# Kernel optimization log

Measured on AMD Instinct MI355X. Metric: run time of the kernel, lower is better.

Reference implementation:

```python
import jax, jax.numpy as jnp
import numpy as np

N_HEADS = 8
FACTOR = 5
N_LAYERS = 2
D_MODEL = 512


def _pos_enc(L, d):
    pos = jnp.arange(L, dtype=jnp.float32)[:, None]
    div = jnp.exp(jnp.arange(0, d, 2, dtype=jnp.float32) * (-np.log(10000.0) / d))
    pe = jnp.zeros((L, d), dtype=jnp.float32)
    pe = pe.at[:, 0::2].set(jnp.sin(pos * div))
    pe = pe.at[:, 1::2].set(jnp.cos(pos * div))
    return pe


def _ln(x, g, b, eps=1e-5):
    mu = x.mean(-1, keepdims=True)
    var = ((x - mu) ** 2).mean(-1, keepdims=True)
    return (x - mu) * jax.lax.rsqrt(var + eps) * g + b


def _token_conv(x, W):
    # x: [B, L, C_in]; W: [d_model, C_in, 3]; circular padding k=3 (Informer TokenEmbedding)
    xt = jnp.transpose(x, (0, 2, 1))
    xt = jnp.concatenate([xt[:, :, -1:], xt, xt[:, :, :1]], axis=-1)
    y = jax.lax.conv_general_dilated(xt, W, (1,), 'VALID', dimension_numbers=('NCH', 'OIH', 'NCH'))
    return jnp.transpose(y, (0, 2, 1))


def _prob_attention(Q, K, V):
    # ProbSparse attention (Informer). Q,K,V: [B,H,L,D]
    B, H, L, D = Q.shape
    ln_L = int(np.ceil(np.log(L)))
    U_part = min(FACTOR * ln_L, L)  # sampled keys per query
    u = min(FACTOR * ln_L, L)       # top queries kept
    idx = jax.random.randint(jax.random.key(42), (L, U_part), 0, L)  # shared across B,H as in torch
    K_sample = K[:, :, idx, :]                                  # [B,H,L,U_part,D]
    QK_sample = jnp.einsum('bhld,bhlud->bhlu', Q, K_sample)
    M = QK_sample.max(-1) - QK_sample.mean(-1)                  # sparsity measure [B,H,L]
    _, M_top = jax.lax.top_k(M, u)                              # [B,H,u]
    Q_reduce = jnp.take_along_axis(Q, M_top[..., None], axis=2) # [B,H,u,D]
    scores = jnp.einsum('bhud,bhld->bhul', Q_reduce, K) / jnp.sqrt(jnp.float32(D))
    attn = jax.nn.softmax(scores, axis=-1)
    ctx = jnp.broadcast_to(V.mean(axis=2, keepdims=True), Q.shape)  # non-selected -> mean(V)
    upd = jnp.einsum('bhul,bhld->bhud', attn, V)
    bi = jnp.arange(B)[:, None, None]
    hi = jnp.arange(H)[None, :, None]
    return ctx.at[bi, hi, M_top].set(upd)                       # scatter selected queries


def reference(x_state_enc, x_enc, x_mark_enc, state_emb_W, token_conv_W, time_W, time_b,
              Wq, bq, Wk, bk, Wv, bv, Wo, bo, ln1_g, ln1_b, ln2_g, ln2_b,
              ffn1_W, ffn1_b, ffn2_W, ffn2_b, norm_g, norm_b):
    B, L = x_state_enc.shape
    dm = D_MODEL
    H = N_HEADS
    dk = dm // H
    # StatePosEmbedding: state emb + token conv emb + time-feature linear + sinusoidal pos
    x = state_emb_W[x_state_enc] + _token_conv(x_enc, token_conv_W) + x_mark_enc @ time_W + time_b + _pos_enc(L, dm)
    for l in range(N_LAYERS):
        q = (x @ Wq[l] + bq[l]).reshape(B, L, H, dk).transpose(0, 2, 1, 3)
        k = (x @ Wk[l] + bk[l]).reshape(B, L, H, dk).transpose(0, 2, 1, 3)
        v = (x @ Wv[l] + bv[l]).reshape(B, L, H, dk).transpose(0, 2, 1, 3)
        ctx = _prob_attention(q, k, v).transpose(0, 2, 1, 3).reshape(B, L, dm)
        x = x + (ctx @ Wo[l] + bo[l])
        x = _ln(x, ln1_g[l], ln1_b[l])
        y = jax.nn.gelu(x @ ffn1_W[l] + ffn1_b[l], approximate=False)
        y = y @ ffn2_W[l] + ffn2_b[l]
        x = _ln(x + y, ln2_g[l], ln2_b[l])
    x = _ln(x, norm_g, norm_b)
    logits = x[:, -1:, :] @ state_emb_W.T  # pred_len = 1
    return logits[:, :, :-1]


def setup_inputs() -> dict:
    key = jax.random.key(0)
    ks = jax.random.split(key, 16)
    B, L, C_IN, MARK = 4, 2048, 7, 4
    NG = 100
    dm, dff, NL = 512, 2048, 2
    s = 0.02
    return {
        'x_state_enc': jax.random.randint(ks[0], (B, L), 0, NG + 1),
        'x_enc': jax.random.normal(ks[1], (B, L, C_IN), dtype=jnp.float32),
        'x_mark_enc': jax.random.normal(ks[2], (B, L, MARK), dtype=jnp.float32),
        'state_emb_W': jax.random.normal(ks[3], (NG + 1, dm), dtype=jnp.float32) * s,
        'token_conv_W': jax.random.normal(ks[4], (dm, C_IN, 3), dtype=jnp.float32) * s,
        'time_W': jax.random.normal(ks[5], (MARK, dm), dtype=jnp.float32) * s,
        'time_b': jnp.zeros((dm,), jnp.float32),
        'Wq': jax.random.normal(ks[6], (NL, dm, dm), dtype=jnp.float32) * s,
        'bq': jnp.zeros((NL, dm), jnp.float32),
        'Wk': jax.random.normal(ks[7], (NL, dm, dm), dtype=jnp.float32) * s,
        'bk': jnp.zeros((NL, dm), jnp.float32),
        'Wv': jax.random.normal(ks[8], (NL, dm, dm), dtype=jnp.float32) * s,
        'bv': jnp.zeros((NL, dm), jnp.float32),
        'Wo': jax.random.normal(ks[9], (NL, dm, dm), dtype=jnp.float32) * s,
        'bo': jnp.zeros((NL, dm), jnp.float32),
        'ln1_g': jnp.ones((NL, dm), jnp.float32),
        'ln1_b': jnp.zeros((NL, dm), jnp.float32),
        'ln2_g': jnp.ones((NL, dm), jnp.float32),
        'ln2_b': jnp.zeros((NL, dm), jnp.float32),
        'ffn1_W': jax.random.normal(ks[10], (NL, dm, dff), dtype=jnp.float32) * s,
        'ffn1_b': jnp.zeros((NL, dff), jnp.float32),
        'ffn2_W': jax.random.normal(ks[11], (NL, dff, dm), dtype=jnp.float32) * s,
        'ffn2_b': jnp.zeros((NL, dm), jnp.float32),
        'norm_g': jnp.ones((dm,), jnp.float32),
        'norm_b': jnp.zeros((dm,), jnp.float32),
    }
```

## Files before the change

kernel.cpp:

```cpp
#include <hip/hip_runtime.h>
#include <hip/hip_bf16.h>

#define L_SEQ 2048
#define NB    4
#define DM    512
#define NH    8
#define DK    64
#define DFF   2048
#define NSAMP 40
#define NGRID 100
#define PARTC 16
#define CKEY  128

typedef __attribute__((ext_vector_type(8))) short bf16x8;
typedef __attribute__((ext_vector_type(4))) float f32x4;

__device__ __forceinline__ unsigned rotl32(unsigned x, unsigned r){ return (x<<r)|(x>>(32u-r)); }
__device__ __forceinline__ float bf2f(ushort u){ return __uint_as_float(((unsigned)u)<<16); }
__device__ __forceinline__ ushort f2bf(float f){
  unsigned u = __float_as_uint(f);
  unsigned r = (u + 0x7fffu + ((u>>16)&1u)) >> 16;
  return (ushort)r;
}

__device__ __forceinline__ void threefry2x32(unsigned k0, unsigned k1, unsigned x0, unsigned x1,
                                             unsigned &o0, unsigned &o1){
  unsigned ks0=k0, ks1=k1, ks2=k0^k1^0x1BD11BDAu;
  x0 += ks0; x1 += ks1;
#define RND(r) { x0 += x1; x1 = rotl32(x1, r); x1 ^= x0; }
  RND(13u) RND(15u) RND(26u) RND(6u)   x0+=ks1; x1+=ks2+1u;
  RND(17u) RND(29u) RND(16u) RND(24u)  x0+=ks2; x1+=ks0+2u;
  RND(13u) RND(15u) RND(26u) RND(6u)   x0+=ks0; x1+=ks1+3u;
  RND(17u) RND(29u) RND(16u) RND(24u)  x0+=ks1; x1+=ks2+4u;
  RND(13u) RND(15u) RND(26u) RND(6u)   x0+=ks2; x1+=ks0+5u;
#undef RND
  o0=x0; o1=x1;
}

__global__ __launch_bounds__(256) void k_prep(
    const float* __restrict__ Wq, const float* __restrict__ Wk,
    const float* __restrict__ Wv, const float* __restrict__ Wo,
    const float* __restrict__ f1W, const float* __restrict__ f2W,
    const float* __restrict__ bq, const float* __restrict__ bk, const float* __restrict__ bv,
    ushort* __restrict__ wt, float* __restrict__ bcat, int* __restrict__ sidx)
{
  const size_t F1T=1048576, F2T=2097152, LSTR=3145728;
  int bid = blockIdx.x, t = threadIdx.x;
  if (bid >= 6145){
    int i = (bid-6145)*256 + t;
    const int total = L_SEQ*NSAMP;
    if (i < total){
      unsigned o0, o1;
      threefry2x32(0u, 42u, 0u, (unsigned)(total + i), o0, o1);
      sidx[i] = (int)((o0 ^ o1) & (unsigned)(L_SEQ-1));
    }
    return;
  }
  if (bid == 6144){
    for (int i=t; i<2*1536; i+=256){
      int l = i / 1536, r = i - l*1536;
      float v = (r<512) ? bq[l*DM+r] : (r<1024) ? bk[l*DM+r-512] : bv[l*DM+r-1024];
      bcat[i] = v;
    }
    return;
  }
  int l = bid >= 3072; bid -= l*3072;
  const float* src; ushort* dst; int K, N, tile;
  if (bid < 1024){
    int m = bid >> 8; tile = bid & 255;
    src = (m==0?Wq:m==1?Wk:m==2?Wv:Wo) + (size_t)l*DM*DM;
    dst = wt + (size_t)l*LSTR + (size_t)m*262144; K=DM; N=DM;
  } else if (bid < 2048){
    tile = bid-1024; src = f1W + (size_t)l*DM*DFF; dst = wt + (size_t)l*LSTR + F1T; K=DM; N=DFF;
  } else {
    tile = bid-2048; src = f2W + (size_t)l*DFF*DM; dst = wt + (size_t)l*LSTR + F2T; K=DFF; N=DM;
  }
  int ntn = N/32;
  int n0 = (tile % ntn)*32, k0 = (tile / ntn)*32;
  __shared__ float tl[32][33];
  int r = t >> 5, c = t & 31;
  for (int rr=r; rr<32; rr+=8) tl[rr][c] = src[(size_t)(k0+rr)*N + n0 + c];
  __syncthreads();
  for (int rr=r; rr<32; rr+=8)
    dst[(size_t)(n0+rr)*K + k0 + c] = f2bf(tl[c][rr]);
}

__global__ __launch_bounds__(256) void k_embed(const int* __restrict__ tok,
    const float* __restrict__ x_enc, const float* __restrict__ x_mark,
    const float* __restrict__ embW, const float* __restrict__ convW,
    const float* __restrict__ timeW, const float* __restrict__ timeb,
    float* __restrict__ x, ushort* __restrict__ xb){
  int bl = blockIdx.x; int b = bl >> 11; int l = bl & (L_SEQ-1);
  __shared__ float xin[21];
  __shared__ float xm[4];
  int t = threadIdx.x;
  if (t < 21){
    int tt = t/7, i = t - tt*7;
    int ll = (l + tt - 1) & (L_SEQ-1);
    xin[t] = x_enc[((size_t)b*L_SEQ + ll)*7 + i];
  }
  if (t >= 32 && t < 36) xm[t-32] = x_mark[((size_t)b*L_SEQ + l)*4 + (t-32)];
  __syncthreads();
  int tk = tok[bl];
  #pragma unroll
  for (int rep=0; rep<2; rep++){
    int d = t + rep*256;
    float v = embW[(size_t)tk*DM + d];
    const float* w = convW + (size_t)d*21;
    float cv = 0.f;
    #pragma unroll
    for (int tt=0; tt<3; tt++)
      #pragma unroll
      for (int i=0; i<7; i++)
        cv = fmaf(xin[tt*7+i], w[i*3+tt], cv);
    v += cv;
    float tv = timeb[d];
    #pragma unroll
    for (int m=0; m<4; m++) tv = fmaf(xm[m], timeW[m*DM + d], tv);
    v += tv;
    int j = d >> 1;
    float div = expf((float)(2*j) * (-0.017988946039015984f));
    float ang = (float)l * div;
    v += (d & 1) ? cosf(ang) : sinf(ang);
    x[(size_t)bl*DM + d] = v;
    xb[(size_t)bl*DM + d] = f2bf(v);
  }
}

enum { MG_ADD=0, MG_GELU_BF16=1, MG_QKV=2 };

__global__ __launch_bounds__(256) void k_mgemm(
    const ushort* __restrict__ A, const ushort* __restrict__ Bt,
    const float* __restrict__ bias, float* __restrict__ Cf,
    ushort* __restrict__ Cb, int M, int N, int K, int mode)
{
  __shared__ ushort As[64][64];
  __shared__ ushort Bs[64][64];
  int tid = threadIdx.x, lane = tid & 63, wid = tid >> 6;
  int nwg = gridDim.x*gridDim.y;
  int id  = blockIdx.y*gridDim.x + blockIdx.x;
  int sid = (id & 7)*(nwg >> 3) + (id >> 3);
  int bx = sid % gridDim.x, by = sid / gridDim.x;
  int m0 = by*64, n0 = bx*64;
  int wr = wid >> 1, wc = wid & 1;
  f32x4 acc[2][2];
  #pragma unroll
  for (int i=0;i<2;i++)
    #pragma unroll
    for(int j=0;j<2;j++) acc[i][j] = (f32x4){0.f,0.f,0.f,0.f};

  for (int k0 = 0; k0 < K; k0 += 64){
    __syncthreads();
    #pragma unroll
    for (int it=0; it<2; it++){
      int e   = it*256 + tid;
      int row = e >> 3, seg = e & 7;
      int gseg = seg ^ (row & 7);
      __builtin_amdgcn_global_load_lds(
        (const __attribute__((address_space(1))) void*)(A + (size_t)(m0+row)*K + k0 + gseg*8),
        (__attribute__((address_space(3))) void*)(&As[0][0] + (size_t)e*8), 16, 0, 0);
      __builtin_amdgcn_global_load_lds(
        (const __attribute__((address_space(1))) void*)(Bt + (size_t)(n0+row)*K + k0 + gseg*8),
        (__attribute__((address_space(3))) void*)(&Bs[0][0] + (size_t)e*8), 16, 0, 0);
    }
    __syncthreads();
    #pragma unroll
    for (int kk=0; kk<2; kk++){
      bf16x8 af[2], bfv[2];
      int seg = kk*4 + (lane>>4);
      #pragma unroll
      for (int i=0;i<2;i++){
        int row = wr*32 + i*16 + (lane&15);
        af[i]  = *(const bf16x8*)&As[row][(seg ^ (row&7))*8];
      }
      #pragma unroll
      for (int j=0;j<2;j++){
        int row = wc*32 + j*16 + (lane&15);
        bfv[j] = *(const bf16x8*)&Bs[row][(seg ^ (row&7))*8];
      }
      #pragma unroll
      for (int i=0;i<2;i++)
        #pragma unroll
        for (int j=0;j<2;j++)
          acc[i][j] = __builtin_amdgcn_mfma_f32_16x16x32_bf16(af[i], bfv[j], acc[i][j], 0,0,0);
    }
  }

  int fq = lane >> 4, fr = lane & 15;
  for (int i=0;i<2;i++){
    for (int j=0;j<2;j++){
      #pragma unroll
      for (int jj=0;jj<4;jj++){
        int r = m0 + wr*32 + i*16 + fq*4 + jj;
        int c = n0 + wc*32 + j*16 + fr;
        float v = acc[i][j][jj] + bias[c];
        if (mode == MG_ADD){
          Cf[(size_t)r*N + c] += v;
        } else if (mode == MG_GELU_BF16){
          float g = 0.5f*v*(1.f + erff(v*0.70710678118654752f));
          Cb[(size_t)r*N + c] = f2bf(g);
        } else {
          int b = r >> 11, l = r & (L_SEQ-1), m3 = c >> 9, hh = (c>>6)&7, d = c & 63;
          Cb[(size_t)m3*4194304 + (((size_t)b*NH + hh)*L_SEQ + l)*64 + d] = f2bf(v);
        }
      }
    }
  }
}

__global__ __launch_bounds__(256) void k_vmean1(const ushort* __restrict__ V, float* __restrict__ part){
  int blk = blockIdx.x;
  int bh = blk >> 5, ch = blk & 31;
  int t = threadIdx.x, d = t & 63, c = t >> 6;
  const ushort* Vb = V + (size_t)bh*L_SEQ*DK + (size_t)(ch*64 + c*16)*DK;
  float s = 0.f;
  #pragma unroll
  for (int r=0; r<16; r++) s += bf2f(Vb[r*DK + d]);
  __shared__ float red[256];
  red[t]=s; __syncthreads();
  if (t < 64) part[(size_t)blk*64 + t] = red[t]+red[t+64]+red[t+128]+red[t+192];
}
__global__ __launch_bounds__(64) void k_vmean2(const float* __restrict__ part, float* __restrict__ vmean){
  int bh = blockIdx.x, d = threadIdx.x;
  float s = 0.f;
  #pragma unroll
  for (int ch=0; ch<32; ch++) s += part[(size_t)(bh*32+ch)*64 + d];
  vmean[bh*64+d] = s * (1.f/(float)L_SEQ);
}

__global__ __launch_bounds__(256) void k_mscore(const ushort* __restrict__ Q, const ushort* __restrict__ Km,
    const int* __restrict__ idx, float* __restrict__ M){
  int wid = threadIdx.x >> 6, lane = threadIdx.x & 63;
  int g = blockIdx.x*4 + wid;
  int l = g & (L_SEQ-1), bh = g >> 11;
  int sg = lane >> 3, dg = lane & 7;

  bf16x8 qv = *(const bf16x8*)(Q + (size_t)g*64 + dg*8);
  float qf[8];
  #pragma unroll
  for (int e=0;e<8;e++) qf[e] = bf2f((ushort)qv[e]);

  const int* ir = idx + l*NSAMP;
  int ki[5];
  #pragma unroll
  for (int i=0;i<5;i++) ki[i] = ir[i*8 + sg];
  const ushort* Kb = Km + (size_t)bh*L_SEQ*64;
  bf16x8 kv[5];
  #pragma unroll
  for (int i=0;i<5;i++) kv[i] = *(const bf16x8*)(Kb + (size_t)ki[i]*64 + dg*8);

  float mx = -INFINITY, sm = 0.f;
  #pragma unroll
  for (int i=0;i<5;i++){
    float d = 0.f;
    #pragma unroll
    for (int e=0;e<8;e++) d = fmaf(qf[e], bf2f((ushort)kv[i][e]), d);
    #pragma unroll
    for (int off=1; off<8; off<<=1) d += __shfl_xor(d, off);
    mx = fmaxf(mx, d);
    sm += d;
  }
  #pragma unroll
  for (int off=1; off<64; off<<=1){
    mx = fmaxf(mx, __shfl_xor(mx, off));
    sm += __shfl_xor(sm, off);
  }
  if (lane==0) M[g] = mx - sm * (1.f/(8.f*(float)NSAMP));
}

__global__ __launch_bounds__(64) void k_topk(const float* __restrict__ M, int* __restrict__ Mtop){
  int bh = blockIdx.x, lane = threadIdx.x;
  float v[32];
  #pragma unroll
  for (int s=0; s<32; s++) v[s] = M[(size_t)bh*L_SEQ + s*64 + lane];
  for (int sel=0; sel<NSAMP; sel++){
    float best = -INFINITY; int bs = 0;
    #pragma unroll
    for (int s=0; s<32; s++){
      if (v[s] > best){ best = v[s]; bs = s; }
    }
    int bidx = bs*64 + lane;
    #pragma unroll
    for (int off=1; off<64; off<<=1){
      float ov = __shfl_xor(best, off);
      int   oi = __shfl_xor(bidx, off);
      if (ov > best || (ov == best && oi < bidx)){ best = ov; bidx = oi; }
    }
    if (lane == 0) Mtop[bh*NSAMP + sel] = bidx;
    int cs = bidx >> 6, cl = bidx & 63;
    if (lane == cl){
      #pragma unroll
      for (int s=0; s<32; s++) if (s == cs) v[s] = -INFINITY;
    }
  }
}

__global__ __launch_bounds__(256) void k_ctxfill(const float* __restrict__ vmean, ushort* __restrict__ ctx){
  int i = blockIdx.x*256 + threadIdx.x;
  int c = i & (DM-1);
  int b = i >> 20;
  int h = c >> 6, d = c & 63;
  ctx[i] = f2bf(vmean[((b<<3)+h)*64 + d]);
}

__global__ __launch_bounds__(256) void k_attn1(const ushort* __restrict__ Q, const ushort* __restrict__ K,
    const ushort* __restrict__ V, const int* __restrict__ Mtop,
    float* __restrict__ pm, float* __restrict__ ps, float* __restrict__ pO){
  int bid = blockIdx.x;
  int xcd = bid & 7, idx = bid >> 3;
  int bh = xcd*4 + (idx & 3), ch = idx >> 2;
  int l0 = ch * CKEY;
  int t = threadIdx.x, lane = t & 63, w = t >> 6;

  __shared__ ushort Qs[48][64];
  __shared__ ushort Ks[CKEY][64];
  __shared__ ushort Vs[CKEY][66];
  __shared__ ushort Ps[48][136];
  __shared__ float rmax[4][48];
  __shared__ float rsum[4][48];
  __shared__ float Oacc[48][64];
  __shared__ int qidx[48];

  if (t < 40) qidx[t] = Mtop[bh*NSAMP + t];
  const ushort* Kb = K + ((size_t)bh*L_SEQ + l0)*64;
  #pragma unroll
  for (int i=0;i<4;i++){
    int e = i*256 + t;
    __builtin_amdgcn_global_load_lds(
      (const __attribute__((address_space(1))) void*)(Kb + (size_t)e*8),
      (__attribute__((address_space(3))) void*)(&Ks[0][0] + (size_t)e*8), 16, 0, 0);
  }
  __syncthreads();

  const ushort* Qb = Q + (size_t)bh*L_SEQ*64;
  {
    int row = t >> 3, seg = t & 7;
    bf16x8 qv = *(const bf16x8*)(Qb + (size_t)qidx[row]*64 + seg*8);
    *(bf16x8*)&Qs[row][seg*8] = qv;
    if (t < 128){
      int r2 = 32 + (t>>3);
      bf16x8 z = (bf16x8){0,0,0,0,0,0,0,0};
      if (r2 < 40) z = *(const bf16x8*)(Qb + (size_t)qidx[r2]*64 + (t&7)*8);
      *(bf16x8*)&Qs[r2][(t&7)*8] = z;
    }
  }
  const ushort* Vb = V + ((size_t)bh*L_SEQ + l0)*64;
  #pragma unroll
  for (int i=0;i<4;i++){
    int e = i*256 + t;
    int row = e >> 3, seg = e & 7;
    bf16x8 vv = *(const bf16x8*)(Vb + (size_t)e*8);
    *(bf16x8*)&Vs[row][seg*8] = vv;
  }
  __syncthreads();

  for (int i=t; i<48*64; i+=256) ((float*)Oacc)[i] = 0.f;

  f32x4 sa[3][2];
  #pragma unroll
  for (int i=0;i<3;i++) for (int j=0;j<2;j++) sa[i][j] = (f32x4){0.f,0.f,0.f,0.f};
  #pragma unroll
  for (int ks=0; ks<2; ks++){
    int ko = ks*32 + (lane>>4)*8;
    bf16x8 af[3], bf[2];
    #pragma unroll
    for (int i=0;i<3;i++) af[i] = *(const bf16x8*)&Qs[i*16 + (lane&15)][ko];
    #pragma unroll
    for (int j=0;j<2;j++) bf[j] = *(const bf16x8*)&Ks[w*32 + j*16 + (lane&15)][ko];
    #pragma unroll
    for (int i=0;i<3;i++)
      #pragma unroll
      for (int j=0;j<2;j++)
        sa[i][j] = __builtin_amdgcn_mfma_f32_16x16x32_bf16(af[i], bf[j], sa[i][j], 0,0,0);
  }
  #pragma unroll
  for (int i=0;i<3;i++)
    #pragma unroll
    for (int j=0;j<2;j++)
      #pragma unroll
      for (int jj=0;jj<4;jj++) sa[i][j][jj] *= 0.125f;
  #pragma unroll
  for (int i=0;i<3;i++){
    #pragma unroll
    for (int jj=0;jj<4;jj++){
      float mx = fmaxf(sa[i][0][jj], sa[i][1][jj]);
      #pragma unroll
      for (int off=1; off<16; off<<=1) mx = fmaxf(mx, __shfl_xor(mx, off));
      if ((lane&15)==0) rmax[w][i*16 + (lane>>4)*4 + jj] = mx;
    }
  }
  __syncthreads();
  #pragma unroll
  for (int i=0;i<3;i++){
    #pragma unroll
    for (int jj=0;jj<4;jj++){
      int row = i*16 + (lane>>4)*4 + jj;
      float m = fmaxf(fmaxf(rmax[0][row], rmax[1][row]), fmaxf(rmax[2][row], rmax[3][row]));
      float p0 = __expf(sa[i][0][jj] - m);
      float p1 = __expf(sa[i][1][jj] - m);
      Ps[row][w*32 + (lane&15)]      = f2bf(p0);
      Ps[row][w*32 + 16 + (lane&15)] = f2bf(p1);
      float sm = p0 + p1;
      #pragma unroll
      for (int off=1; off<16; off<<=1) sm += __shfl_xor(sm, off);
      if ((lane&15)==0) rsum[w][row] = sm;
    }
  }
  __syncthreads();

  f32x4 oa[3][4];
  #pragma unroll
  for (int i=0;i<3;i++) for (int j=0;j<4;j++) oa[i][j] = (f32x4){0.f,0.f,0.f,0.f};
  {
    bf16x8 pa[3], vb[4];
    int kbase = w*32 + (lane>>4)*8;
    #pragma unroll
    for (int i=0;i<3;i++) pa[i] = *(const bf16x8*)&Ps[i*16 + (lane&15)][kbase];
    #pragma unroll
    for (int j=0;j<4;j++){
      #pragma unroll
      for (int e=0;e<8;e++) vb[j][e] = (short)Vs[kbase + e][j*16 + (lane&15)];
    }
    #pragma unroll
    for (int i=0;i<3;i++)
      #pragma unroll
      for (int j=0;j<4;j++)
        oa[i][j] = __builtin_amdgcn_mfma_f32_16x16x32_bf16(pa[i], vb[j], oa[i][j], 0,0,0);
  }
  #pragma unroll
  for (int ww=0; ww<4; ww++){
    if (w == ww){
      #pragma unroll
      for (int i=0;i<3;i++)
        #pragma unroll
        for (int j=0;j<4;j++)
          #pragma unroll
          for (int jj=0;jj<4;jj++)
            Oacc[i*16 + (lane>>4)*4 + jj][j*16 + (lane&15)] += oa[i][j][jj];
    }
    __syncthreads();
  }

  size_t base = ((size_t)bh*PARTC + ch);
  if (t < 40){
    float m = fmaxf(fmaxf(rmax[0][t], rmax[1][t]), fmaxf(rmax[2][t], rmax[3][t]));
    pm[base*40 + t] = m;
    ps[base*40 + t] = rsum[0][t]+rsum[1][t]+rsum[2][t]+rsum[3][t];
  }
  {
    int row = t >> 3, d0 = (t&7)*8;
    float* dst = pO + (base*48 + row)*64 + d0;
    #pragma unroll
    for (int e=0;e<8;e++) dst[e] = Oacc[row][d0+e];
    if (t < 64){
      int r2 = 32 + (t>>3);
      float* dst2 = pO + (base*48 + r2)*64 + d0;
      #pragma unroll
      for (int e=0;e<8;e++) dst2[e] = Oacc[r2][d0+e];
    }
  }
}

__global__ __launch_bounds__(256) void k_attn2(const float* __restrict__ pm, const float* __restrict__ ps,
    const float* __restrict__ pO, const int* __restrict__ Mtop, ushort* __restrict__ ctx){
  int bh = blockIdx.x, b = bh >> 3, h = bh & 7;
  int t = threadIdx.x;
  __shared__ float wch[PARTC][40];
  __shared__ float inv_s[40];
  __shared__ int qidx[40];
  if (t < 40){
    qidx[t] = Mtop[bh*NSAMP + t];
    float m = -INFINITY;
    #pragma unroll
    for (int c=0;c<PARTC;c++) m = fmaxf(m, pm[((size_t)bh*PARTC + c)*40 + t]);
    float s = 0.f;
    #pragma unroll
    for (int c=0;c<PARTC;c++){
      float wc = __expf(pm[((size_t)bh*PARTC + c)*40 + t] - m);
      wch[c][t] = wc;
      s += wc * ps[((size_t)bh*PARTC + c)*40 + t];
    }
    inv_s[t] = 1.f / s;
  }
  __syncthreads();
  #pragma unroll
  for (int iter=0; iter<2; iter++){
    int row = iter*32 + (t>>3);
    if (row < 40){
      int d0 = (t&7)*8;
      float o[8] = {0.f,0.f,0.f,0.f,0.f,0.f,0.f,0.f};
      for (int c=0;c<PARTC;c++){
        const float* pp = pO + (((size_t)bh*PARTC + c)*48 + row)*64 + d0;
        float wc = wch[c][row];
        float4 a = *(const float4*)pp, b4 = *(const float4*)(pp+4);
        o[0]=fmaf(wc,a.x,o[0]); o[1]=fmaf(wc,a.y,o[1]); o[2]=fmaf(wc,a.z,o[2]); o[3]=fmaf(wc,a.w,o[3]);
        o[4]=fmaf(wc,b4.x,o[4]); o[5]=fmaf(wc,b4.y,o[5]); o[6]=fmaf(wc,b4.z,o[6]); o[7]=fmaf(wc,b4.w,o[7]);
      }
      float is = inv_s[row];
      bf16x8 wv;
      #pragma unroll
      for (int e=0;e<8;e++) wv[e] = (short)f2bf(o[e]*is);
      *(bf16x8*)(ctx + ((size_t)b*L_SEQ + qidx[row])*DM + h*64 + d0) = wv;
    }
  }
}

__global__ __launch_bounds__(256) void k_ln(float* __restrict__ x,
    const float* __restrict__ g, const float* __restrict__ b,
    ushort* __restrict__ xb){
  int row = blockIdx.x*4 + (threadIdx.x>>6);
  int lane = threadIdx.x & 63;
  float* xr = x + (size_t)row*DM + lane*8;
  float4 v0 = *(const float4*)(xr);
  float4 v1 = *(const float4*)(xr + 4);
  float s = v0.x+v0.y+v0.z+v0.w+v1.x+v1.y+v1.z+v1.w;
  #pragma unroll
  for (int off=1; off<64; off<<=1) s += __shfl_xor(s, off);
  float mu = s * (1.f/(float)DM);
  float d0=v0.x-mu, d1=v0.y-mu, d2=v0.z-mu, d3=v0.w-mu;
  float d4=v1.x-mu, d5=v1.y-mu, d6=v1.z-mu, d7=v1.w-mu;
  float q = d0*d0+d1*d1+d2*d2+d3*d3+d4*d4+d5*d5+d6*d6+d7*d7;
  #pragma unroll
  for (int off=1; off<64; off<<=1) q += __shfl_xor(q, off);
  float r = rsqrtf(q * (1.f/(float)DM) + 1e-5f);
  float4 g0 = *(const float4*)(g + lane*8);
  float4 g1 = *(const float4*)(g + lane*8 + 4);
  float4 b0 = *(const float4*)(b + lane*8);
  float4 b1 = *(const float4*)(b + lane*8 + 4);
  float o0=d0*r*g0.x+b0.x, o1=d1*r*g0.y+b0.y, o2=d2*r*g0.z+b0.z, o3=d3*r*g0.w+b0.w;
  float o4=d4*r*g1.x+b1.x, o5=d5*r*g1.y+b1.y, o6=d6*r*g1.z+b1.z, o7=d7*r*g1.w+b1.w;
  *(float4*)(xr)     = (float4){o0,o1,o2,o3};
  *(float4*)(xr + 4) = (float4){o4,o5,o6,o7};
  if (xb){
    bf16x8 w;
    w[0]=(short)f2bf(o0); w[1]=(short)f2bf(o1); w[2]=(short)f2bf(o2); w[3]=(short)f2bf(o3);
    w[4]=(short)f2bf(o4); w[5]=(short)f2bf(o5); w[6]=(short)f2bf(o6); w[7]=(short)f2bf(o7);
    *(bf16x8*)(xb + (size_t)row*DM + lane*8) = w;
  }
}

__global__ __launch_bounds__(64) void k_logits(const float* __restrict__ x, const float* __restrict__ embW,
                                               float* __restrict__ out){
  int bid = blockIdx.x;
  int b = bid / NGRID, g = bid - b*NGRID;
  const float* xr = x + ((size_t)b*L_SEQ + (L_SEQ-1))*DM;
  const float* er = embW + (size_t)g*DM;
  int lane = threadIdx.x;
  float s = 0.f;
  for (int d=lane; d<DM; d+=64) s = fmaf(xr[d], er[d], s);
  for (int off=32; off; off>>=1) s += __shfl_xor(s, off);
  if (lane==0) out[bid] = s;
}

extern "C" void kernel_launch(void* const* d_in, const int* in_sizes, int n_in,
                              void* d_out, int out_size, void* d_ws, size_t ws_size,
                              hipStream_t stream) {
  const int*   tok    = (const int*)d_in[0];
  const float* x_enc  = (const float*)d_in[1];
  const float* x_mark = (const float*)d_in[2];
  const float* embW   = (const float*)d_in[3];
  const float* convW  = (const float*)d_in[4];
  const float* timeW  = (const float*)d_in[5];
  const float* timeb  = (const float*)d_in[6];
  const float* Wq = (const float*)d_in[7];  const float* bq = (const float*)d_in[8];
  const float* Wk = (const float*)d_in[9];  const float* bk = (const float*)d_in[10];
  const float* Wv = (const float*)d_in[11]; const float* bv = (const float*)d_in[12];
  const float* Wo = (const float*)d_in[13]; const float* bo = (const float*)d_in[14];
  const float* ln1g = (const float*)d_in[15]; const float* ln1b = (const float*)d_in[16];
  const float* ln2g = (const float*)d_in[17]; const float* ln2b = (const float*)d_in[18];
  const float* f1W = (const float*)d_in[19]; const float* f1b = (const float*)d_in[20];
  const float* f2W = (const float*)d_in[21]; const float* f2b = (const float*)d_in[22];
  const float* nrmg = (const float*)d_in[23]; const float* nrmb = (const float*)d_in[24];
  float* out = (float*)d_out;

  char* ws = (char*)d_ws;
  float*  x    = (float*) (ws);
  ushort* xb   = (ushort*)(ws + ((size_t)16<<20));
  ushort* q    = (ushort*)(ws + ((size_t)24<<20));
  ushort* kbuf = (ushort*)(ws + ((size_t)32<<20));
  ushort* vbuf = (ushort*)(ws + ((size_t)40<<20));
  ushort* ctx  = (ushort*)(ws + ((size_t)48<<20));
  ushort* hbuf = (ushort*)(ws + ((size_t)24<<20));
  ushort* wt   = (ushort*)(ws + ((size_t)56<<20));
  float*  Mbuf = (float*) (ws + ((size_t)69<<20));
  int*    Mtop = (int*)   (ws + ((size_t)70<<20));
  int*    sidx = (int*)   (ws + ((size_t)71<<20));
  float*  vmean= (float*) (ws + ((size_t)72<<20));
  float*  bcat = (float*) (ws + ((size_t)73<<20));
  float*  part = (float*) (ws + ((size_t)74<<20));
  float*  pO   = (float*) (ws + ((size_t)75<<20));
  float*  pmb  = (float*) (ws + ((size_t)82<<20));
  float*  psb  = (float*) (ws + ((size_t)82<<20) + 102400);

  const int Mrows = NB*L_SEQ;
  const size_t WQT=0, WOT=786432, F1T=1048576, F2T=2097152, LSTR=3145728;

  k_prep<<<6465, 256, 0, stream>>>(Wq, Wk, Wv, Wo, f1W, f2W, bq, bk, bv, wt, bcat, sidx);
  k_embed<<<NB*L_SEQ, 256, 0, stream>>>(tok, x_enc, x_mark, embW, convW, timeW, timeb, x, xb);

  for (int l=0; l<2; l++){
    size_t b5 = (size_t)l*DM;
    ushort* wl = wt + (size_t)l*LSTR;

    k_mgemm<<<dim3(1536/64, Mrows/64), 256, 0, stream>>>(xb, wl+WQT, bcat+l*1536, nullptr, q, Mrows, 1536, DM, MG_QKV);
    k_vmean1<<<NB*NH*32, 256, 0, stream>>>(vbuf, part);
    k_vmean2<<<NB*NH, 64, 0, stream>>>(part, vmean);
    k_mscore<<<NB*NH*L_SEQ/4, 256, 0, stream>>>(q, kbuf, sidx, Mbuf);
    k_topk<<<NB*NH, 64, 0, stream>>>(Mbuf, Mtop);
    k_ctxfill<<<(NB*L_SEQ*DM)/256, 256, 0, stream>>>(vmean, ctx);
    k_attn1<<<NB*NH*PARTC, 256, 0, stream>>>(q, kbuf, vbuf, Mtop, pmb, psb, pO);
    k_attn2<<<NB*NH, 256, 0, stream>>>(pmb, psb, pO, Mtop, ctx);
    k_mgemm<<<dim3(DM/64, Mrows/64), 256, 0, stream>>>(ctx, wl+WOT, bo+b5, x, nullptr, Mrows, DM, DM, MG_ADD);
    k_ln<<<Mrows/4, 256, 0, stream>>>(x, ln1g+b5, ln1b+b5, xb);
    k_mgemm<<<dim3(DFF/64, Mrows/64), 256, 0, stream>>>(xb, wl+F1T, f1b + (size_t)l*DFF, nullptr, hbuf, Mrows, DFF, DM, MG_GELU_BF16);
    k_mgemm<<<dim3(DM/64, Mrows/64), 256, 0, stream>>>(hbuf, wl+F2T, f2b+b5, x, nullptr, Mrows, DM, DFF, MG_ADD);
    k_ln<<<Mrows/4, 256, 0, stream>>>(x, ln2g+b5, ln2b+b5, xb);
  }
  k_ln<<<Mrows/4, 256, 0, stream>>>(x, nrmg, nrmb, nullptr);
  k_logits<<<NB*NGRID, 64, 0, stream>>>(x, embW, out);
}
```

Measured before the change: 518.7 us.

## Split top-k selection into two-stage per-slice candidate pass and merge

The single-block-per-head top-k over 2048 scores is replaced by a first kernel in which 8 blocks per head each pick the top 40 from a 256-element slice, followed by a merge kernel that selects the final 40 from the 320 candidates. Values and indices are packed into one 64-bit sortable key (order-preserving float bits plus inverted index), so each reduction step needs a single shuffle-max instead of separate value and index shuffles with tie handling. This spreads the serial 40-round selection across more wavefronts to use more of the GPU, at the cost of one extra launch and a small candidate buffer in global memory.

```diff
diff --git a/kernel.cpp b/kernel.cpp
--- a/kernel.cpp
+++ b/kernel.cpp
@@ -21,6 +21,10 @@
   unsigned u = __float_as_uint(f);
   unsigned r = (u + 0x7fffu + ((u>>16)&1u)) >> 16;
   return (ushort)r;
+}
+__device__ __forceinline__ unsigned fkey(float f){
+  unsigned u = __float_as_uint(f);
+  return (u & 0x80000000u) ? ~u : (u | 0x80000000u);
 }
 
 __device__ __forceinline__ void threefry2x32(unsigned k0, unsigned k1, unsigned x0, unsigned x1,
@@ -268,30 +272,53 @@
   if (lane==0) M[g] = mx - sm * (1.f/(8.f*(float)NSAMP));
 }
 
-__global__ __launch_bounds__(64) void k_topk(const float* __restrict__ M, int* __restrict__ Mtop){
+__global__ __launch_bounds__(64) void k_topk1(const float* __restrict__ M,
+                                              unsigned long long* __restrict__ cand){
+  int blk = blockIdx.x;
+  int bh = blk >> 3, sl = blk & 7;
+  int lane = threadIdx.x;
+  const float* Mr = M + (size_t)bh*L_SEQ + sl*256;
+  unsigned long long k[4];
+  #pragma unroll
+  for (int s=0; s<4; s++){
+    int j = s*64 + lane;
+    int gidx = sl*256 + j;
+    k[s] = ((unsigned long long)fkey(Mr[j]) << 32) | (unsigned)(~gidx);
+  }
+  for (int sel=0; sel<NSAMP; sel++){
+    unsigned long long best = k[0];
+    #pragma unroll
+    for (int s=1; s<4; s++) best = (k[s] > best) ? k[s] : best;
+    #pragma unroll
+    for (int off=1; off<64; off<<=1){
+      unsigned long long o = __shfl_xor(best, off);
+      best = (o > best) ? o : best;
+    }
+    #pragma unroll
+    for (int s=0; s<4; s++) if (k[s] == best) k[s] = 0ull;
+    if (lane == 0) cand[(size_t)blk*NSAMP + sel] = best;
+  }
+}
+
+__global__ __launch_bounds__(64) void k_topk2(const unsigned long long* __restrict__ cand,
+                                              int* __restrict__ Mtop){
   int bh = blockIdx.x, lane = threadIdx.x;
-  float v[32];
-  #pragma unroll
-  for (int s=0; s<32; s++) v[s] = M[(size_t)bh*L_SEQ + s*64 + lane];
+  const unsigned long long* cb = cand + (size_t)bh*8*NSAMP;
+  unsigned long long k[5];
+  #pragma unroll
+  for (int s=0; s<5; s++) k[s] = cb[s*64 + lane];
   for (int sel=0; sel<NSAMP; sel++){
-    float best = -INFINITY; int bs = 0;
-    #pragma unroll
-    for (int s=0; s<32; s++){
-      if (v[s] > best){ best = v[s]; bs = s; }
-    }
-    int bidx = bs*64 + lane;
+    unsigned long long best = k[0];
+    #pragma unroll
+    for (int s=1; s<5; s++) best = (k[s] > best) ? k[s] : best;
     #pragma unroll
     for (int off=1; off<64; off<<=1){
-      float ov = __shfl_xor(best, off);
-      int   oi = __shfl_xor(bidx, off);
-      if (ov > best || (ov == best && oi < bidx)){ best = ov; bidx = oi; }
-    }
-    if (lane == 0) Mtop[bh*NSAMP + sel] = bidx;
-    int cs = bidx >> 6, cl = bidx & 63;
-    if (lane == cl){
-      #pragma unroll
-      for (int s=0; s<32; s++) if (s == cs) v[s] = -INFINITY;
-    }
+      unsigned long long o = __shfl_xor(best, off);
+      best = (o > best) ? o : best;
+    }
+    #pragma unroll
+    for (int s=0; s<5; s++) if (k[s] == best) k[s] = 0ull;
+    if (lane == 0) Mtop[bh*NSAMP + sel] = (int)(~(unsigned)best & (L_SEQ-1));
   }
 }
 
@@ -591,6 +618,7 @@
   float*  pO   = (float*) (ws + ((size_t)75<<20));
   float*  pmb  = (float*) (ws + ((size_t)82<<20));
   float*  psb  = (float*) (ws + ((size_t)82<<20) + 102400);
+  unsigned long long* cand = (unsigned long long*)(ws + ((size_t)83<<20));
 
   const int Mrows = NB*L_SEQ;
   const size_t WQT=0, WOT=786432, F1T=1048576, F2T=2097152, LSTR=3145728;
@@ -606,7 +634,8 @@
     k_vmean1<<<NB*NH*32, 256, 0, stream>>>(vbuf, part);
     k_vmean2<<<NB*NH, 64, 0, stream>>>(part, vmean);
     k_mscore<<<NB*NH*L_SEQ/4, 256, 0, stream>>>(q, kbuf, sidx, Mbuf);
-    k_topk<<<NB*NH, 64, 0, stream>>>(Mbuf, Mtop);
+    k_topk1<<<NB*NH*8, 64, 0, stream>>>(Mbuf, cand);
+    k_topk2<<<NB*NH, 64, 0, stream>>>(cand, Mtop);
     k_ctxfill<<<(NB*L_SEQ*DM)/256, 256, 0, stream>>>(vmean, ctx);
     k_attn1<<<NB*NH*PARTC, 256, 0, stream>>>(q, kbuf, vbuf, Mtop, pmb, psb, pO);
     k_attn2<<<NB*NH, 256, 0, stream>>>(pmb, psb, pO, Mtop, ctx);
```

After: 494.7 us. 4.6% less time.
